# Kernel tuning notes

Measured on AMD Instinct MI355X. Metric: run time of the kernel, lower is better.

Reference implementation:

```python
import jax, jax.numpy as jnp
import numpy as np

U, I, D, K, L, E = 100000, 50000, 64, 128, 2, 1250000
N = U + I
EPS = 1e-12


def setup_inputs() -> dict:
    key = jax.random.key(0)
    ks = jax.random.split(key, 8)
    return {
        "user_emb": jax.random.normal(ks[0], (U, D), jnp.float32) * 0.1,
        "item_emb": jax.random.normal(ks[1], (I, D), jnp.float32) * 0.1,
        "user_intent": jax.random.normal(ks[2], (D, K), jnp.float32) * 0.1,
        "item_intent": jax.random.normal(ks[3], (D, K), jnp.float32) * 0.1,
        "adj_vals": jax.random.uniform(ks[4], (E,), jnp.float32) * 0.1,
        "h_idx": jax.random.randint(ks[5], (E,), 0, N, jnp.int32),
        "t_idx": jax.random.randint(ks[6], (E,), 0, N, jnp.int32),
        "users": jax.random.randint(ks[7], (1024,), 0, U, jnp.int32),
        "items": jax.random.randint(jax.random.fold_in(key, 9), (1024,), 0, I, jnp.int32),
    }


def _l2norm(x):
    # torch F.normalize(p=2, dim=1): x / max(||x||_2, eps)
    n = jnp.sqrt(jnp.sum(x * x, axis=1, keepdims=True))
    return x / jnp.maximum(n, EPS)


def reference(user_emb, item_emb, user_intent, item_intent, adj_vals, h_idx, t_idx, users, items):
    n_users = user_emb.shape[0]
    n_nodes = n_users + item_emb.shape[0]

    def spmm(vals, x):
        # sparse [N,N] @ dense [N,D] via edge gather + segment-sum scatter
        return jax.ops.segment_sum(vals[:, None] * x[t_idx], h_idx, num_segments=n_nodes)

    def adaptive_vals(head, tail):
        hn, tn = _l2norm(head), _l2norm(tail)
        edge_alpha = (jnp.sum(hn * tn, axis=1) + 1.0) * 0.5  # [E]
        row_sum = jax.ops.segment_sum(edge_alpha, h_idx, num_segments=n_nodes)  # dense row-sum equivalent
        d_inv = jnp.where(row_sum > 0, 1.0 / row_sum, 0.0)
        return d_inv[h_idx] * edge_alpha  # G edge values

    all_emb = [jnp.concatenate([user_emb, item_emb], axis=0)]  # [N, D]
    gnn_list, int_list, gaa_list, iaa_list = [], [], [], []
    for _ in range(L):
        ek = all_emb[-1]
        gnn = spmm(adj_vals, ek)
        u_e, i_e = ek[:n_users], ek[n_users:]
        u_int = jax.nn.softmax(u_e @ user_intent, axis=1) @ user_intent.T
        i_int = jax.nn.softmax(i_e @ item_intent, axis=1) @ item_intent.T
        intl = jnp.concatenate([u_int, i_int], axis=0)
        g_graph = adaptive_vals(gnn[h_idx], gnn[t_idx])
        g_inten = adaptive_vals(intl[h_idx], intl[t_idx])
        gaa = spmm(g_graph, ek)
        iaa = spmm(g_inten, ek)
        gnn_list.append(gnn); int_list.append(intl)
        gaa_list.append(gaa); iaa_list.append(iaa)
        all_emb.append(gnn + intl + gaa + iaa + ek)

    final = jnp.sum(jnp.stack(all_emb, axis=1), axis=1)  # [N, D]
    ua, ia = final[:n_users], final[n_users:]
    return (ua, ia, jnp.stack(gnn_list), jnp.stack(int_list), jnp.stack(gaa_list), jnp.stack(iaa_list))
```

## Files before the change

kernel.cpp:

```cpp
#include <hip/hip_runtime.h>


#define U_CNT 100000
#define I_CNT 50000
#define D_DIM 64
#define K_DIM 128
#define L_LAYERS 2
#define E_CNT 1250000
#define N_CNT (U_CNT + I_CNT)
#define EPSF 1e-12f

#define UBLK ((U_CNT + 63) / 64)
#define IBLK ((I_CNT + 63) / 64)

__device__ __forceinline__ float wave_sum(float v) {
#pragma unroll
  for (int off = 32; off > 0; off >>= 1) v += __shfl_xor(v, off, 64);
  return v;
}

__global__ void init_kernel(const float* __restrict__ ue, const float* __restrict__ ie,
                            float* __restrict__ ek, float* __restrict__ fin) {
  int idx = blockIdx.x * blockDim.x + threadIdx.x;
  const int total = N_CNT * D_DIM;
  for (; idx < total; idx += gridDim.x * blockDim.x) {
    float v = (idx < U_CNT * D_DIM) ? ue[idx] : ie[idx - U_CNT * D_DIM];
    ek[idx] = v;
    fin[idx] = v;
  }
}

__global__ void hist_kernel(const int* __restrict__ h_idx, int* __restrict__ counts) {
  int e = blockIdx.x * blockDim.x + threadIdx.x;
  for (; e < E_CNT; e += gridDim.x * blockDim.x) atomicAdd(&counts[h_idx[e]], 1);
}

__global__ void scan_kernel(const int* __restrict__ counts, int* __restrict__ row_ptr,
                            int* __restrict__ cursor) {
  __shared__ int wsum[16];
  __shared__ int s_carry, s_total;
  int tid = threadIdx.x, lane = tid & 63, wv = tid >> 6;
  if (tid == 0) s_carry = 0;
  __syncthreads();
  for (int base = 0; base < N_CNT; base += 4096) {
    int idx = base + tid * 4;
    int v0 = (idx + 0 < N_CNT) ? counts[idx + 0] : 0;
    int v1 = (idx + 1 < N_CNT) ? counts[idx + 1] : 0;
    int v2 = (idx + 2 < N_CNT) ? counts[idx + 2] : 0;
    int v3 = (idx + 3 < N_CNT) ? counts[idx + 3] : 0;
    int s = v0 + v1 + v2 + v3;
    int x = s;
#pragma unroll
    for (int off = 1; off < 64; off <<= 1) {
      int y = __shfl_up(x, off, 64);
      if (lane >= off) x += y;
    }
    if (lane == 63) wsum[wv] = x;
    __syncthreads();
    if (wv == 0 && lane < 16) {
      int w = wsum[lane];
      int xx = w;
#pragma unroll
      for (int off = 1; off < 16; off <<= 1) {
        int y = __shfl_up(xx, off, 64);
        if (lane >= off) xx += y;
      }
      wsum[lane] = xx - w;
      if (lane == 15) s_total = xx;
    }
    __syncthreads();
    int carry = s_carry;
    int e0 = carry + wsum[wv] + (x - s);
    int e1 = e0 + v0, e2 = e1 + v1, e3 = e2 + v2;
    if (idx + 0 < N_CNT) { row_ptr[idx + 0] = e0; cursor[idx + 0] = e0; }
    if (idx + 1 < N_CNT) { row_ptr[idx + 1] = e1; cursor[idx + 1] = e1; }
    if (idx + 2 < N_CNT) { row_ptr[idx + 2] = e2; cursor[idx + 2] = e2; }
    if (idx + 3 < N_CNT) { row_ptr[idx + 3] = e3; cursor[idx + 3] = e3; }
    __syncthreads();
    if (tid == 0) s_carry = carry + s_total;
    __syncthreads();
  }
  if (threadIdx.x == 0) row_ptr[N_CNT] = s_carry;
}

__global__ void scatter_kernel(const int* __restrict__ h_idx, const int* __restrict__ t_idx,
                               const float* __restrict__ adj_vals, int* __restrict__ cursor,
                               int* __restrict__ t_sorted, float* __restrict__ v_sorted) {
  int e = blockIdx.x * blockDim.x + threadIdx.x;
  for (; e < E_CNT; e += gridDim.x * blockDim.x) {
    int h = h_idx[e];
    int pos = atomicAdd(&cursor[h], 1);
    t_sorted[pos] = t_idx[e];
    v_sorted[pos] = adj_vals[e];
  }
}

__global__ void transposeW_kernel(const float* __restrict__ Wu, const float* __restrict__ Wi,
                                  float* __restrict__ WuT, float* __restrict__ WiT) {
  int idx = blockIdx.x * blockDim.x + threadIdx.x;
  for (; idx < 2 * D_DIM * K_DIM; idx += gridDim.x * blockDim.x) {
    int w = idx >> 13, r = idx & (D_DIM * K_DIM - 1);
    int d = r >> 7, k = r & (K_DIM - 1);
    const float* W = w ? Wi : Wu;
    float* WT = w ? WiT : WuT;
    WT[k * D_DIM + d] = W[d * K_DIM + k];
  }
}

__global__ void spmm_gnn_kernel(const float* __restrict__ ek, const int* __restrict__ t_sorted,
                                const float* __restrict__ v_sorted,
                                const int* __restrict__ row_ptr, float* __restrict__ gnn,
                                float* __restrict__ invn_g) {
  int wv = threadIdx.x >> 6, lane = threadIdx.x & 63;
  int slot = lane >> 4, f = (lane & 15) << 2;
  int n = blockIdx.x * 4 + wv;
  if (n >= N_CNT) return;
  int start = row_ptr[n], end = row_ptr[n + 1];
  float ax = 0.f, ay = 0.f, az = 0.f, aw = 0.f;
  for (int i = start; i < end; i += 4) {
    int idx = i + slot;
    int ic = (idx < end) ? idx : (end - 1);
    int t = t_sorted[ic];
    float v = v_sorted[ic];
    if (idx >= end) v = 0.f;
    const float4 x = *(const float4*)(ek + (size_t)t * D_DIM + f);
    ax = fmaf(v, x.x, ax);
    ay = fmaf(v, x.y, ay);
    az = fmaf(v, x.z, az);
    aw = fmaf(v, x.w, aw);
  }
#pragma unroll
  for (int off = 16; off <= 32; off <<= 1) {
    ax += __shfl_xor(ax, off, 64);
    ay += __shfl_xor(ay, off, 64);
    az += __shfl_xor(az, off, 64);
    aw += __shfl_xor(aw, off, 64);
  }
  if (slot == 0) {
    float4 o = make_float4(ax, ay, az, aw);
    *(float4*)(gnn + (size_t)n * D_DIM + f) = o;
  }
  float ss = ax * ax + ay * ay + az * az + aw * aw;
#pragma unroll
  for (int off = 1; off <= 8; off <<= 1) ss += __shfl_xor(ss, off, 64);
  if (lane == 0) invn_g[n] = 1.f / fmaxf(sqrtf(ss), EPSF);
}

__global__ __launch_bounds__(64) void intent_kernel(
    const float* __restrict__ ek, const float* __restrict__ Wu, const float* __restrict__ WuT,
    const float* __restrict__ Wi, const float* __restrict__ WiT, float* __restrict__ intl,
    float* __restrict__ invn_i) {
  __shared__ float T[D_DIM * 65];
  const int lane = threadIdx.x;
  const int b = blockIdx.x;
  int n0, cnt;
  const float *W, *WT;
  if (b < UBLK) {
    n0 = b * 64;
    cnt = (U_CNT - n0 < 64) ? (U_CNT - n0) : 64;
    W = Wu;
    WT = WuT;
  } else {
    n0 = U_CNT + (b - UBLK) * 64;
    cnt = (N_CNT - n0 < 64) ? (N_CNT - n0) : 64;
    W = Wi;
    WT = WiT;
  }
  const int h = lane >> 4, m = lane & 15;

#pragma unroll
  for (int i = 0; i < 16; i++) {
    int r = i * 4 + h;
    float4 v = make_float4(0.f, 0.f, 0.f, 0.f);
    if (r < cnt) v = *(const float4*)(ek + (size_t)(n0 + r) * D_DIM + m * 4);
    T[(4 * m + 0) * 65 + r] = v.x;
    T[(4 * m + 1) * 65 + r] = v.y;
    T[(4 * m + 2) * 65 + r] = v.z;
    T[(4 * m + 3) * 65 + r] = v.w;
  }
  __syncthreads();

  float a[K_DIM];
#pragma unroll
  for (int k = 0; k < K_DIM; k++) a[k] = 0.f;
#pragma unroll 2
  for (int d = 0; d < D_DIM; d++) {
    float ed = T[d * 65 + lane];
    const float* __restrict__ wr = W + d * K_DIM;
#pragma unroll
    for (int k = 0; k < K_DIM; k++) a[k] = fmaf(wr[k], ed, a[k]);
  }

  float m0 = a[0], m1 = a[1], m2 = a[2], m3 = a[3];
#pragma unroll
  for (int k = 4; k < K_DIM; k += 4) {
    m0 = fmaxf(m0, a[k]);
    m1 = fmaxf(m1, a[k + 1]);
    m2 = fmaxf(m2, a[k + 2]);
    m3 = fmaxf(m3, a[k + 3]);
  }
  float mx = fmaxf(fmaxf(m0, m1), fmaxf(m2, m3));
  float s0 = 0.f, s1 = 0.f, s2 = 0.f, s3 = 0.f;
#pragma unroll
  for (int k = 0; k < K_DIM; k += 4) {
    a[k] = __expf(a[k] - mx);
    s0 += a[k];
    a[k + 1] = __expf(a[k + 1] - mx);
    s1 += a[k + 1];
    a[k + 2] = __expf(a[k + 2] - mx);
    s2 += a[k + 2];
    a[k + 3] = __expf(a[k + 3] - mx);
    s3 += a[k + 3];
  }
  float inv_s = 1.f / ((s0 + s1) + (s2 + s3));

  float o[D_DIM];
#pragma unroll
  for (int d = 0; d < D_DIM; d++) o[d] = 0.f;

  __syncthreads();
#pragma unroll
  for (int k = 0; k < 64; k++) T[k * 65 + lane] = a[k];
  __syncthreads();
#pragma unroll 2
  for (int k = 0; k < 64; k++) {
    float pk = T[k * 65 + lane];
    const float* __restrict__ wr = WT + k * D_DIM;
#pragma unroll
    for (int d = 0; d < D_DIM; d++) o[d] = fmaf(wr[d], pk, o[d]);
  }
  __syncthreads();
#pragma unroll
  for (int k = 0; k < 64; k++) T[k * 65 + lane] = a[k + 64];
  __syncthreads();
#pragma unroll 2
  for (int k = 0; k < 64; k++) {
    float pk = T[k * 65 + lane];
    const float* __restrict__ wr = WT + (k + 64) * D_DIM;
#pragma unroll
    for (int d = 0; d < D_DIM; d++) o[d] = fmaf(wr[d], pk, o[d]);
  }

  float ns = 0.f;
#pragma unroll
  for (int d = 0; d < D_DIM; d++) {
    o[d] *= inv_s;
    ns = fmaf(o[d], o[d], ns);
  }
  if (lane < cnt) invn_i[n0 + lane] = 1.f / fmaxf(sqrtf(ns), EPSF);

  __syncthreads();
#pragma unroll
  for (int d = 0; d < D_DIM; d++) T[d * 65 + lane] = o[d];
  __syncthreads();
#pragma unroll
  for (int i = 0; i < 16; i++) {
    int r = i * 4 + h;
    if (r < cnt) {
      float4 v = make_float4(T[(4 * m + 0) * 65 + r], T[(4 * m + 1) * 65 + r],
                             T[(4 * m + 2) * 65 + r], T[(4 * m + 3) * 65 + r]);
      *(float4*)(intl + (size_t)(n0 + r) * D_DIM + m * 4) = v;
    }
  }
}

__global__ void passB_kernel(const float* __restrict__ ek, const float* __restrict__ gnn,
                             const float* __restrict__ intl, const float* __restrict__ invn_g,
                             const float* __restrict__ invn_i, const int* __restrict__ t_sorted,
                             const int* __restrict__ row_ptr, float* __restrict__ gaa,
                             float* __restrict__ iaa, float* __restrict__ ek_next,
                             float* __restrict__ fin) {
  int wv = threadIdx.x >> 6, lane = threadIdx.x & 63;
  int slot = lane >> 4, f = (lane & 15) << 2;
  int n = blockIdx.x * 4 + wv;
  if (n >= N_CNT) return;
  int start = row_ptr[n], end = row_ptr[n + 1];
  const float4 gh = *(const float4*)(gnn + (size_t)n * D_DIM + f);
  const float4 ih = *(const float4*)(intl + (size_t)n * D_DIM + f);
  float ig = invn_g[n], ii = invn_i[n];
  float rs_g = 0.f, rs_i = 0.f;
  float gx = 0.f, gy = 0.f, gz = 0.f, gw = 0.f;
  float ix = 0.f, iy = 0.f, iz = 0.f, iw = 0.f;
  for (int i = start; i < end; i += 4) {
    int idx = i + slot;
    int ic = (idx < end) ? idx : (end - 1);
    int t = t_sorted[ic];
    size_t rb = (size_t)t * D_DIM + f;
    const float4 gt = *(const float4*)(gnn + rb);
    const float4 it = *(const float4*)(intl + rb);
    const float4 et = *(const float4*)(ek + rb);
    float ivg = invn_g[t];
    float ivi = invn_i[t];
    float dg = gh.x * gt.x + gh.y * gt.y + gh.z * gt.z + gh.w * gt.w;
    float di = ih.x * it.x + ih.y * it.y + ih.z * it.z + ih.w * it.w;
#pragma unroll
    for (int off = 1; off <= 8; off <<= 1) {
      dg += __shfl_xor(dg, off, 64);
      di += __shfl_xor(di, off, 64);
    }
    float ag = fmaf(dg * ig, ivg, 1.f) * 0.5f;
    float ai = fmaf(di * ii, ivi, 1.f) * 0.5f;
    if (idx >= end) { ag = 0.f; ai = 0.f; }
    rs_g += ag;
    rs_i += ai;
    gx = fmaf(ag, et.x, gx);
    gy = fmaf(ag, et.y, gy);
    gz = fmaf(ag, et.z, gz);
    gw = fmaf(ag, et.w, gw);
    ix = fmaf(ai, et.x, ix);
    iy = fmaf(ai, et.y, iy);
    iz = fmaf(ai, et.z, iz);
    iw = fmaf(ai, et.w, iw);
  }
#pragma unroll
  for (int off = 16; off <= 32; off <<= 1) {
    rs_g += __shfl_xor(rs_g, off, 64);
    rs_i += __shfl_xor(rs_i, off, 64);
    gx += __shfl_xor(gx, off, 64);
    gy += __shfl_xor(gy, off, 64);
    gz += __shfl_xor(gz, off, 64);
    gw += __shfl_xor(gw, off, 64);
    ix += __shfl_xor(ix, off, 64);
    iy += __shfl_xor(iy, off, 64);
    iz += __shfl_xor(iz, off, 64);
    iw += __shfl_xor(iw, off, 64);
  }
  float dgi = (rs_g > 0.f) ? 1.f / rs_g : 0.f;
  float dii = (rs_i > 0.f) ? 1.f / rs_i : 0.f;
  if (slot == 0) {
    size_t ob = (size_t)n * D_DIM + f;
    float4 ga = make_float4(gx * dgi, gy * dgi, gz * dgi, gw * dgi);
    float4 ia = make_float4(ix * dii, iy * dii, iz * dii, iw * dii);
    *(float4*)(gaa + ob) = ga;
    *(float4*)(iaa + ob) = ia;
    const float4 eh = *(const float4*)(ek + ob);
    float4 en = make_float4(gh.x + ih.x + ga.x + ia.x + eh.x, gh.y + ih.y + ga.y + ia.y + eh.y,
                            gh.z + ih.z + ga.z + ia.z + eh.z, gh.w + ih.w + ga.w + ia.w + eh.w);
    *(float4*)(ek_next + ob) = en;
    float4 fo = *(const float4*)(fin + ob);
    fo.x += en.x;
    fo.y += en.y;
    fo.z += en.z;
    fo.w += en.w;
    *(float4*)(fin + ob) = fo;
  }
}

extern "C" void kernel_launch(void* const* d_in, const int* in_sizes, int n_in, void* d_out,
                              int out_size, void* d_ws, size_t ws_size, hipStream_t stream) {
  const float* user_emb = (const float*)d_in[0];
  const float* item_emb = (const float*)d_in[1];
  const float* user_intent = (const float*)d_in[2];
  const float* item_intent = (const float*)d_in[3];
  const float* adj_vals = (const float*)d_in[4];
  const int* h_idx = (const int*)d_in[5];
  const int* t_idx = (const int*)d_in[6];

  float* out = (float*)d_out;
  float* fin = out;
  float* gnn_base = out + (size_t)N_CNT * D_DIM;
  float* intl_base = gnn_base + (size_t)L_LAYERS * N_CNT * D_DIM;
  float* gaa_base = intl_base + (size_t)L_LAYERS * N_CNT * D_DIM;
  float* iaa_base = gaa_base + (size_t)L_LAYERS * N_CNT * D_DIM;

  float* ws = (float*)d_ws;
  float* ekA = ws;
  float* ekB = ekA + (size_t)N_CNT * D_DIM;
  float* v_sorted = ekB + (size_t)N_CNT * D_DIM;
  float* invn_g = v_sorted + E_CNT;
  float* invn_i = invn_g + N_CNT;
  int* t_sorted = (int*)(invn_i + N_CNT);
  int* row_ptr = t_sorted + E_CNT;
  int* counts = row_ptr + (N_CNT + 1);
  int* cursor = counts + N_CNT;
  float* wtu = (float*)(cursor + N_CNT);
  float* wti = wtu + (size_t)D_DIM * K_DIM;

  hipMemsetAsync(counts, 0, N_CNT * sizeof(int), stream);
  init_kernel<<<2048, 256, 0, stream>>>(user_emb, item_emb, ekA, fin);
  hist_kernel<<<2048, 256, 0, stream>>>(h_idx, counts);
  transposeW_kernel<<<32, 512, 0, stream>>>(user_intent, item_intent, wtu, wti);
  scan_kernel<<<1, 1024, 0, stream>>>(counts, row_ptr, cursor);
  scatter_kernel<<<2048, 256, 0, stream>>>(h_idx, t_idx, adj_vals, cursor, t_sorted, v_sorted);

  float* ek = ekA;
  float* ekn = ekB;
  const int nodeBlocks = (N_CNT + 3) / 4;
  const int intentBlocks = UBLK + IBLK;
  for (int l = 0; l < L_LAYERS; l++) {
    float* gnn = gnn_base + (size_t)l * N_CNT * D_DIM;
    float* intl = intl_base + (size_t)l * N_CNT * D_DIM;
    float* gaa = gaa_base + (size_t)l * N_CNT * D_DIM;
    float* iaa = iaa_base + (size_t)l * N_CNT * D_DIM;
    spmm_gnn_kernel<<<nodeBlocks, 256, 0, stream>>>(ek, t_sorted, v_sorted, row_ptr, gnn, invn_g);
    intent_kernel<<<intentBlocks, 64, 0, stream>>>(ek, user_intent, wtu, item_intent, wti, intl,
                                                   invn_i);
    passB_kernel<<<nodeBlocks, 256, 0, stream>>>(ek, gnn, intl, invn_g, invn_i, t_sorted, row_ptr,
                                                 gaa, iaa, ekn, fin);
    float* tmp = ek;
    ek = ekn;
    ekn = tmp;
  }
}
```

Before: 1.370 ms.

## Parallelize CSR scan, drop redundant fin traffic, use nontemporal stores

Replaces the single-block prefix scan with a three-kernel multi-block scan (block partials, scan of partials, local scan). Instead of writing and read-modify-writing the running final sum every layer, the final output is computed once in the last layer from ek0 + ek1 + ek2, and the last layer skips writing ek_next. Output-only arrays (gaa, iaa, fin) use nontemporal stores to reduce cache pollution. The intent kernel gets a min-blocks launch bound, and an extra workspace buffer keeps the original embeddings alive.

```diff
diff --git a/kernel.cpp b/kernel.cpp
--- a/kernel.cpp
+++ b/kernel.cpp
@@ -13,20 +13,28 @@
 #define UBLK ((U_CNT + 63) / 64)
 #define IBLK ((I_CNT + 63) / 64)
 
-__device__ __forceinline__ float wave_sum(float v) {
-#pragma unroll
-  for (int off = 32; off > 0; off >>= 1) v += __shfl_xor(v, off, 64);
-  return v;
+#define SC_BLOCKS 256
+#define SC_TPB 256
+#define SC_CHUNK ((N_CNT + SC_BLOCKS - 1) / SC_BLOCKS)
+
+typedef float vfloat4 __attribute__((ext_vector_type(4)));
+
+__device__ __forceinline__ void nt_store4(float* p, float4 v) {
+  vfloat4 nv;
+  nv.x = v.x;
+  nv.y = v.y;
+  nv.z = v.z;
+  nv.w = v.w;
+  __builtin_nontemporal_store(nv, (vfloat4*)p);
 }
 
 __global__ void init_kernel(const float* __restrict__ ue, const float* __restrict__ ie,
-                            float* __restrict__ ek, float* __restrict__ fin) {
+                            float* __restrict__ ek) {
   int idx = blockIdx.x * blockDim.x + threadIdx.x;
   const int total = N_CNT * D_DIM;
   for (; idx < total; idx += gridDim.x * blockDim.x) {
     float v = (idx < U_CNT * D_DIM) ? ue[idx] : ie[idx - U_CNT * D_DIM];
     ek[idx] = v;
-    fin[idx] = v;
   }
 }
 
@@ -35,52 +43,69 @@
   for (; e < E_CNT; e += gridDim.x * blockDim.x) atomicAdd(&counts[h_idx[e]], 1);
 }
 
-__global__ void scan_kernel(const int* __restrict__ counts, int* __restrict__ row_ptr,
-                            int* __restrict__ cursor) {
-  __shared__ int wsum[16];
-  __shared__ int s_carry, s_total;
+__global__ void scanA_kernel(const int* __restrict__ counts, int* __restrict__ partial) {
+  int b = blockIdx.x, tid = threadIdx.x, lane = tid & 63, wv = tid >> 6;
+  int lo = b * SC_CHUNK;
+  int hi = lo + SC_CHUNK;
+  if (hi > N_CNT) hi = N_CNT;
+  int s = 0;
+  for (int i = lo + tid; i < hi; i += SC_TPB) s += counts[i];
+#pragma unroll
+  for (int off = 32; off > 0; off >>= 1) s += __shfl_xor(s, off, 64);
+  __shared__ int ws[4];
+  if (lane == 0) ws[wv] = s;
+  __syncthreads();
+  if (tid == 0) partial[b] = ws[0] + ws[1] + ws[2] + ws[3];
+}
+
+__global__ void scanB_kernel(const int* __restrict__ partial, int* __restrict__ offs) {
   int tid = threadIdx.x, lane = tid & 63, wv = tid >> 6;
-  if (tid == 0) s_carry = 0;
-  __syncthreads();
-  for (int base = 0; base < N_CNT; base += 4096) {
-    int idx = base + tid * 4;
-    int v0 = (idx + 0 < N_CNT) ? counts[idx + 0] : 0;
-    int v1 = (idx + 1 < N_CNT) ? counts[idx + 1] : 0;
-    int v2 = (idx + 2 < N_CNT) ? counts[idx + 2] : 0;
-    int v3 = (idx + 3 < N_CNT) ? counts[idx + 3] : 0;
-    int s = v0 + v1 + v2 + v3;
-    int x = s;
+  int v = partial[tid];
+  int x = v;
+#pragma unroll
+  for (int off = 1; off < 64; off <<= 1) {
+    int y = __shfl_up(x, off, 64);
+    if (lane >= off) x += y;
+  }
+  __shared__ int wt[4];
+  if (lane == 63) wt[wv] = x;
+  __syncthreads();
+  int add = 0;
+  for (int w = 0; w < wv; w++) add += wt[w];
+  offs[tid] = add + x - v;
+}
+
+__global__ void scanC_kernel(const int* __restrict__ counts, const int* __restrict__ offs,
+                             int* __restrict__ row_ptr, int* __restrict__ cursor) {
+  int b = blockIdx.x, tid = threadIdx.x, lane = tid & 63, wv = tid >> 6;
+  __shared__ int wt[4];
+  int lo = b * SC_CHUNK;
+  int hi = lo + SC_CHUNK;
+  if (hi > N_CNT) hi = N_CNT;
+  int carry = offs[b];
+  for (int base = lo; base < hi; base += SC_TPB) {
+    int i = base + tid;
+    int v = (i < hi) ? counts[i] : 0;
+    int x = v;
 #pragma unroll
     for (int off = 1; off < 64; off <<= 1) {
       int y = __shfl_up(x, off, 64);
       if (lane >= off) x += y;
     }
-    if (lane == 63) wsum[wv] = x;
+    if (lane == 63) wt[wv] = x;
     __syncthreads();
-    if (wv == 0 && lane < 16) {
-      int w = wsum[lane];
-      int xx = w;
-#pragma unroll
-      for (int off = 1; off < 16; off <<= 1) {
-        int y = __shfl_up(xx, off, 64);
-        if (lane >= off) xx += y;
-      }
-      wsum[lane] = xx - w;
-      if (lane == 15) s_total = xx;
-    }
+    int add = carry;
+    for (int w = 0; w < wv; w++) add += wt[w];
+    if (i < hi) {
+      int e = add + x - v;
+      row_ptr[i] = e;
+      cursor[i] = e;
+    }
+    int tot = wt[0] + wt[1] + wt[2] + wt[3];
     __syncthreads();
-    int carry = s_carry;
-    int e0 = carry + wsum[wv] + (x - s);
-    int e1 = e0 + v0, e2 = e1 + v1, e3 = e2 + v2;
-    if (idx + 0 < N_CNT) { row_ptr[idx + 0] = e0; cursor[idx + 0] = e0; }
-    if (idx + 1 < N_CNT) { row_ptr[idx + 1] = e1; cursor[idx + 1] = e1; }
-    if (idx + 2 < N_CNT) { row_ptr[idx + 2] = e2; cursor[idx + 2] = e2; }
-    if (idx + 3 < N_CNT) { row_ptr[idx + 3] = e3; cursor[idx + 3] = e3; }
-    __syncthreads();
-    if (tid == 0) s_carry = carry + s_total;
-    __syncthreads();
-  }
-  if (threadIdx.x == 0) row_ptr[N_CNT] = s_carry;
+    carry += tot;
+  }
+  if (b == 0 && tid == 0) row_ptr[N_CNT] = E_CNT;
 }
 
 __global__ void scatter_kernel(const int* __restrict__ h_idx, const int* __restrict__ t_idx,
@@ -146,7 +171,7 @@
   if (lane == 0) invn_g[n] = 1.f / fmaxf(sqrtf(ss), EPSF);
 }
 
-__global__ __launch_bounds__(64) void intent_kernel(
+__global__ __launch_bounds__(64, 2) void intent_kernel(
     const float* __restrict__ ek, const float* __restrict__ Wu, const float* __restrict__ WuT,
     const float* __restrict__ Wi, const float* __restrict__ WiT, float* __restrict__ intl,
     float* __restrict__ invn_i) {
@@ -264,12 +289,13 @@
   }
 }
 
+template <bool LAST>
 __global__ void passB_kernel(const float* __restrict__ ek, const float* __restrict__ gnn,
                              const float* __restrict__ intl, const float* __restrict__ invn_g,
                              const float* __restrict__ invn_i, const int* __restrict__ t_sorted,
                              const int* __restrict__ row_ptr, float* __restrict__ gaa,
                              float* __restrict__ iaa, float* __restrict__ ek_next,
-                             float* __restrict__ fin) {
+                             const float* __restrict__ ek0, float* __restrict__ fin) {
   int wv = threadIdx.x >> 6, lane = threadIdx.x & 63;
   int slot = lane >> 4, f = (lane & 15) << 2;
   int n = blockIdx.x * 4 + wv;
@@ -331,18 +357,19 @@
     size_t ob = (size_t)n * D_DIM + f;
     float4 ga = make_float4(gx * dgi, gy * dgi, gz * dgi, gw * dgi);
     float4 ia = make_float4(ix * dii, iy * dii, iz * dii, iw * dii);
-    *(float4*)(gaa + ob) = ga;
-    *(float4*)(iaa + ob) = ia;
+    nt_store4(gaa + ob, ga);
+    nt_store4(iaa + ob, ia);
     const float4 eh = *(const float4*)(ek + ob);
     float4 en = make_float4(gh.x + ih.x + ga.x + ia.x + eh.x, gh.y + ih.y + ga.y + ia.y + eh.y,
                             gh.z + ih.z + ga.z + ia.z + eh.z, gh.w + ih.w + ga.w + ia.w + eh.w);
-    *(float4*)(ek_next + ob) = en;
-    float4 fo = *(const float4*)(fin + ob);
-    fo.x += en.x;
-    fo.y += en.y;
-    fo.z += en.z;
-    fo.w += en.w;
-    *(float4*)(fin + ob) = fo;
+    if (LAST) {
+      const float4 e0 = *(const float4*)(ek0 + ob);
+      float4 fo = make_float4(e0.x + eh.x + en.x, e0.y + eh.y + en.y, e0.z + eh.z + en.z,
+                              e0.w + eh.w + en.w);
+      nt_store4(fin + ob, fo);
+    } else {
+      *(float4*)(ek_next + ob) = en;
+    }
   }
 }
 
@@ -366,27 +393,33 @@
   float* ws = (float*)d_ws;
   float* ekA = ws;
   float* ekB = ekA + (size_t)N_CNT * D_DIM;
-  float* v_sorted = ekB + (size_t)N_CNT * D_DIM;
+  float* ekC = ekB + (size_t)N_CNT * D_DIM;
+  float* v_sorted = ekC + (size_t)N_CNT * D_DIM;
   float* invn_g = v_sorted + E_CNT;
   float* invn_i = invn_g + N_CNT;
   int* t_sorted = (int*)(invn_i + N_CNT);
   int* row_ptr = t_sorted + E_CNT;
   int* counts = row_ptr + (N_CNT + 1);
   int* cursor = counts + N_CNT;
-  float* wtu = (float*)(cursor + N_CNT);
+  int* partial = cursor + N_CNT;
+  int* offs = partial + SC_BLOCKS;
+  float* wtu = (float*)(offs + SC_BLOCKS);
   float* wti = wtu + (size_t)D_DIM * K_DIM;
 
-  hipMemsetAsync(counts, 0, N_CNT * sizeof(int), stream);
-  init_kernel<<<2048, 256, 0, stream>>>(user_emb, item_emb, ekA, fin);
+  (void)hipMemsetAsync(counts, 0, N_CNT * sizeof(int), stream);
+  init_kernel<<<2048, 256, 0, stream>>>(user_emb, item_emb, ekA);
   hist_kernel<<<2048, 256, 0, stream>>>(h_idx, counts);
   transposeW_kernel<<<32, 512, 0, stream>>>(user_intent, item_intent, wtu, wti);
-  scan_kernel<<<1, 1024, 0, stream>>>(counts, row_ptr, cursor);
+  scanA_kernel<<<SC_BLOCKS, SC_TPB, 0, stream>>>(counts, partial);
+  scanB_kernel<<<1, SC_BLOCKS, 0, stream>>>(partial, offs);
+  scanC_kernel<<<SC_BLOCKS, SC_TPB, 0, stream>>>(counts, offs, row_ptr, cursor);
   scatter_kernel<<<2048, 256, 0, stream>>>(h_idx, t_idx, adj_vals, cursor, t_sorted, v_sorted);
+
+  const int nodeBlocks = (N_CNT + 3) / 4;
+  const int intentBlocks = UBLK + IBLK;
 
   float* ek = ekA;
   float* ekn = ekB;
-  const int nodeBlocks = (N_CNT + 3) / 4;
-  const int intentBlocks = UBLK + IBLK;
   for (int l = 0; l < L_LAYERS; l++) {
     float* gnn = gnn_base + (size_t)l * N_CNT * D_DIM;
     float* intl = intl_base + (size_t)l * N_CNT * D_DIM;
@@ -395,10 +428,15 @@
     spmm_gnn_kernel<<<nodeBlocks, 256, 0, stream>>>(ek, t_sorted, v_sorted, row_ptr, gnn, invn_g);
     intent_kernel<<<intentBlocks, 64, 0, stream>>>(ek, user_intent, wtu, item_intent, wti, intl,
                                                    invn_i);
-    passB_kernel<<<nodeBlocks, 256, 0, stream>>>(ek, gnn, intl, invn_g, invn_i, t_sorted, row_ptr,
-                                                 gaa, iaa, ekn, fin);
-    float* tmp = ek;
-    ek = ekn;
-    ekn = tmp;
-  }
-}
+    if (l == L_LAYERS - 1) {
+      passB_kernel<true><<<nodeBlocks, 256, 0, stream>>>(ek, gnn, intl, invn_g, invn_i, t_sorted,
+                                                         row_ptr, gaa, iaa, nullptr, ekA, fin);
+    } else {
+      passB_kernel<false><<<nodeBlocks, 256, 0, stream>>>(ek, gnn, intl, invn_g, invn_i, t_sorted,
+                                                          row_ptr, gaa, iaa, ekn, nullptr, nullptr);
+      float* tmp = ek;
+      ek = ekn;
+      ekn = (l == 0) ? ekC : tmp;
+    }
+  }
+}
```

New measurement: 1.900 ms. 38.7% more time.
